# Kernel optimization log

Hardware: AMD Instinct MI355X
Metric: run time of the kernel (lower is better)

## Reference

```python
import jax, jax.numpy as jnp
import numpy as np

H = 128  # hidden size
I = 4    # input size
B = 256  # batch
T = 512  # seq len


def setup_inputs() -> dict:
    key = jax.random.key(0)
    ks = jax.random.split(key, 9)
    k = 1.0 / np.sqrt(H)  # PyTorch LSTM init: U(-1/sqrt(H), 1/sqrt(H))
    u = lambda kk, shape: jax.random.uniform(kk, shape, jnp.float32, -k, k)
    return {
        "x": jax.random.normal(ks[0], (B, T, I), jnp.float32),
        "Wih_f": u(ks[1], (4 * H, I)),
        "Whh_f": u(ks[2], (4 * H, H)),
        "bih_f": u(ks[3], (4 * H,)),
        "bhh_f": u(ks[4], (4 * H,)),
        "Wih_b": u(ks[5], (4 * H, I)),
        "Whh_b": u(ks[6], (4 * H, H)),
        "bih_b": u(ks[7], (4 * H,)),
        "bhh_b": u(ks[8], (4 * H,)),
    }


def _lstm_final_h(xt, Wih, Whh, bih, bhh):
    # xt: [T, B, I]. Returns final hidden state h_T: [B, H].
    # Precompute input projection for all timesteps (batched GEMM).
    xw = jnp.einsum("tbi,gi->tbg", xt, Wih) + (bih + bhh)  # [T, B, 4H]
    h0 = jnp.zeros((xt.shape[1], H), xt.dtype)
    c0 = jnp.zeros((xt.shape[1], H), xt.dtype)

    def step(carry, xw_t):
        h, c = carry
        gates = xw_t + h @ Whh.T  # [B, 4H]
        i, f, g, o = jnp.split(gates, 4, axis=-1)  # PyTorch gate order i,f,g,o
        i = jax.nn.sigmoid(i)
        f = jax.nn.sigmoid(f)
        g = jnp.tanh(g)
        o = jax.nn.sigmoid(o)
        c = f * c + i * g
        h = o * jnp.tanh(c)
        return (h, c), None

    (h_T, _), _ = jax.lax.scan(step, (h0, c0), xw)
    return h_T


def reference(x, Wih_f, Whh_f, bih_f, bhh_f, Wih_b, Whh_b, bih_b, bhh_b):
    xt = jnp.swapaxes(x, 0, 1)  # [T, B, I]
    h_fwd = _lstm_final_h(xt, Wih_f, Whh_f, bih_f, bhh_f)          # forward direction
    h_bwd = _lstm_final_h(xt[::-1], Wih_b, Whh_b, bih_b, bhh_b)    # backward direction
    # h_n: [2, B, H] -> transpose(0,1) -> [B, 2, H] -> reshape [B, 2H]
    return jnp.concatenate([h_fwd, h_bwd], axis=-1)
```

## Files before the change

### kernel.cpp

```cpp
#include <hip/hip_runtime.h>
#include <hip/hip_bf16.h>

typedef _Float16 f16;
typedef _Float16 f16x8 __attribute__((ext_vector_type(8)));
typedef _Float16 f16x4 __attribute__((ext_vector_type(4)));
typedef float    f32x4 __attribute__((ext_vector_type(4)));

#define HDIM 128
#define IDIM 4
#define TLEN 512

__device__ __forceinline__ float sigm(float x){
  return 1.0f / (1.0f + __expf(-x));
}
__device__ __forceinline__ float tanh_fast(float x){
  return 1.0f - 2.0f / (1.0f + __expf(2.0f*x));
}

__global__ __launch_bounds__(512, 2) void bilstm_mfma3(
    const float* __restrict__ x,
    const float* __restrict__ Wih_f, const float* __restrict__ Whh_f,
    const float* __restrict__ bih_f, const float* __restrict__ bhh_f,
    const float* __restrict__ Wih_b, const float* __restrict__ Whh_b,
    const float* __restrict__ bih_b, const float* __restrict__ bhh_b,
    float* __restrict__ out)
{
  __shared__ __align__(16) f16 xs16[2][TLEN][IDIM];
  __shared__ __align__(16) f16 ha[2][4][64][8];

  const int tid = threadIdx.x;
  const int w   = tid >> 6;
  const int l   = tid & 63;
  const int c16 = l & 15;
  const int dir = blockIdx.x >> 7;
  const int b0  = (blockIdx.x & 127) * 2;

  const float* Wih = dir ? Wih_b : Wih_f;
  const float* Whh = dir ? Whh_b : Whh_f;
  const float* bih = dir ? bih_b : bih_f;
  const float* bhh = dir ? bhh_b : bhh_f;

  f16x8 bfrag[4][5];
  #pragma unroll
  for (int t = 0; t < 4; ++t){
    const int gn = t*128 + w*16 + c16;
    #pragma unroll
    for (int ks = 0; ks < 4; ++ks){
      const float* p = Whh + gn*HDIM + ks*32 + (l>>4)*8;
      float4 qa = ((const float4*)p)[0];
      float4 qb = ((const float4*)p)[1];
      f16x8 v = { (f16)qa.x,(f16)qa.y,(f16)qa.z,(f16)qa.w,
                  (f16)qb.x,(f16)qb.y,(f16)qb.z,(f16)qb.w };
      bfrag[t][ks] = v;
    }
    f16x8 v4 = (f16x8)(f16)0.0f;
    if (l < 16){
      const float4 wq = *(const float4*)(Wih + gn*IDIM);
      const float bb = bih[gn] + bhh[gn];
      v4[0] = (f16)wq.x; v4[1] = (f16)wq.y;
      v4[2] = (f16)wq.z; v4[3] = (f16)wq.w;
      v4[4] = (f16)bb;
    }
    bfrag[t][4] = v4;
  }
  #pragma unroll
  for (int t = 0; t < 4; ++t)
    #pragma unroll
    for (int ks = 0; ks < 5; ++ks)
      asm("" : "+v"(bfrag[t][ks]));

  {
    const float4* src0 = (const float4*)(x + (size_t)(b0+0)*TLEN*IDIM);
    const float4* src1 = (const float4*)(x + (size_t)(b0+1)*TLEN*IDIM);
    float4 v0 = src0[tid], v1 = src1[tid];
    f16x4 h0 = { (f16)v0.x, (f16)v0.y, (f16)v0.z, (f16)v0.w };
    f16x4 h1 = { (f16)v1.x, (f16)v1.y, (f16)v1.z, (f16)v1.w };
    *(f16x4*)&xs16[0][tid][0] = h0;
    *(f16x4*)&xs16[1][tid][0] = h1;
  }
  {
    int* hz = (int*)ha;
    hz[tid] = 0; hz[tid+512] = 0; hz[tid+1024] = 0; hz[tid+1536] = 0;
  }
  __syncthreads();

  float c = 0.0f, hout = 0.0f;
  const int chainbit = (l >> 4) & 1;
  int tt = dir ? (TLEN-1) : 0;
  const int dt = dir ? -1 : 1;

  const int Gw  = (l >> 4) + ((2*w + (c16 >> 3)) & 3) * 16;
  const int kse = w >> 1;
  const int ew  = c16 & 7;

#define STEP(RB, WB)                                                          \
  {                                                                           \
    f16x8 a0 = *(const f16x8*)&ha[RB][0][l][0];                               \
    f16x8 a1 = *(const f16x8*)&ha[RB][1][l][0];                               \
    f16x8 a2 = *(const f16x8*)&ha[RB][2][l][0];                               \
    f16x8 a3 = *(const f16x8*)&ha[RB][3][l][0];                               \
    f16x4 xq0 = *(const f16x4*)&xs16[0][tt][0];                               \
    f16x4 xq1 = *(const f16x4*)&xs16[1][tt][0];                               \
    f16x4 zq  = (f16x4)(f16)0.0f;                                             \
    f16x4 sel = (l == 0) ? xq0 : ((l == 1) ? xq1 : zq);                       \
    f16x8 a4  = (f16x8)(f16)0.0f;                                             \
    a4[0] = sel[0]; a4[1] = sel[1]; a4[2] = sel[2]; a4[3] = sel[3];           \
    a4[4] = (l < 2) ? (f16)1.0f : (f16)0.0f;                                  \
    f32x4 zero4 = { 0.f, 0.f, 0.f, 0.f };                                     \
    f32x4 acc[4];                                                             \
    _Pragma("unroll")                                                         \
    for (int t = 0; t < 4; ++t){                                              \
      acc[t] = __builtin_amdgcn_mfma_f32_16x16x32_f16(a0, bfrag[t][0], zero4, 0,0,0); \
      acc[t] = __builtin_amdgcn_mfma_f32_16x16x32_f16(a1, bfrag[t][1], acc[t], 0,0,0); \
      acc[t] = __builtin_amdgcn_mfma_f32_16x16x32_f16(a2, bfrag[t][2], acc[t], 0,0,0); \
      acc[t] = __builtin_amdgcn_mfma_f32_16x16x32_f16(a3, bfrag[t][3], acc[t], 0,0,0); \
      acc[t] = __builtin_amdgcn_mfma_f32_16x16x32_f16(a4, bfrag[t][4], acc[t], 0,0,0); \
    }                                                                         \
    float val[4];                                                             \
    _Pragma("unroll")                                                         \
    for (int t = 0; t < 4; ++t){                                              \
      int pv = __builtin_amdgcn_ds_bpermute(c16 << 2, __float_as_int(acc[t].y)); \
      val[t] = chainbit ? __int_as_float(pv) : acc[t].x;                      \
    }                                                                         \
    float iv = sigm(val[0]);                                                  \
    float fv = sigm(val[1]);                                                  \
    float gv = tanh_fast(val[2]);                                             \
    float ov = sigm(val[3]);                                                  \
    c    = fv*c + iv*gv;                                                      \
    hout = ov * tanh_fast(c);                                                 \
    if (l < 32) ha[WB][kse][Gw][ew] = (f16)hout;                              \
    tt += dt;                                                                 \
    __syncthreads();                                                          \
  }

  for (int s = 0; s < TLEN; s += 2){
    STEP(0, 1)
    STEP(1, 0)
  }
#undef STEP

  if (l < 32){
    out[(size_t)(b0 + (l>>4))*(2*HDIM) + dir*HDIM + w*16 + c16] = hout;
  }
}

extern "C" void kernel_launch(void* const* d_in, const int* in_sizes, int n_in,
                              void* d_out, int out_size, void* d_ws, size_t ws_size,
                              hipStream_t stream)
{
  const float* x     = (const float*)d_in[0];
  const float* Wih_f = (const float*)d_in[1];
  const float* Whh_f = (const float*)d_in[2];
  const float* bih_f = (const float*)d_in[3];
  const float* bhh_f = (const float*)d_in[4];
  const float* Wih_b = (const float*)d_in[5];
  const float* Whh_b = (const float*)d_in[6];
  const float* bih_b = (const float*)d_in[7];
  const float* bhh_b = (const float*)d_in[8];

  bilstm_mfma3<<<dim3(256), dim3(512), 0, stream>>>(
      x, Wih_f, Whh_f, bih_f, bhh_f, Wih_b, Whh_b, bih_b, bhh_b,
      (float*)d_out);
}
```

Measured before the change: 437.1 us.

## Split gate tiles across 16 waves with shared-memory gate exchange

Doubles the block to 1024 threads so each wave computes two 16-column gate tiles instead of four. This halves the serial MFMA chain per step. Gate pre-activations now go through a new shared buffer and an extra barrier, so each step has two syncthreads, and the double-buffered hidden state is replaced by a single buffer. MFMA issue is raised in priority with setprio. The aim is lower per-step latency in the recurrence, paid for with an extra block-wide barrier and LDS traffic on every step.

```diff
diff --git a/kernel.cpp b/kernel.cpp
--- a/kernel.cpp
+++ b/kernel.cpp
@@ -17,7 +17,7 @@
   return 1.0f - 2.0f / (1.0f + __expf(2.0f*x));
 }
 
-__global__ __launch_bounds__(512, 2) void bilstm_mfma3(
+__global__ __launch_bounds__(1024, 4) void bilstm_v4(
     const float* __restrict__ x,
     const float* __restrict__ Wih_f, const float* __restrict__ Whh_f,
     const float* __restrict__ bih_f, const float* __restrict__ bhh_f,
@@ -26,12 +26,15 @@
     float* __restrict__ out)
 {
   __shared__ __align__(16) f16 xs16[2][TLEN][IDIM];
-  __shared__ __align__(16) f16 ha[2][4][64][8];
+  __shared__ __align__(16) f16 ha[4][64][8];
+  __shared__ __align__(16) float graw[2][8][16][4];
 
   const int tid = threadIdx.x;
-  const int w   = tid >> 6;
+  const int wid = tid >> 6;
   const int l   = tid & 63;
   const int c16 = l & 15;
+  const int p   = wid & 7;
+  const int r   = wid >> 3;
   const int dir = blockIdx.x >> 7;
   const int b0  = (blockIdx.x & 127) * 2;
 
@@ -40,18 +43,21 @@
   const float* bih = dir ? bih_b : bih_f;
   const float* bhh = dir ? bhh_b : bhh_f;
 
-  f16x8 bfrag[4][5];
+  const int t0 = p + r*16;
+  const int t1 = t0 + 8;
+
+  f16x8 bfrag[2][5];
   #pragma unroll
-  for (int t = 0; t < 4; ++t){
-    const int gn = t*128 + w*16 + c16;
+  for (int q = 0; q < 2; ++q){
+    const int gn = (q ? t1 : t0)*16 + c16;
     #pragma unroll
     for (int ks = 0; ks < 4; ++ks){
-      const float* p = Whh + gn*HDIM + ks*32 + (l>>4)*8;
-      float4 qa = ((const float4*)p)[0];
-      float4 qb = ((const float4*)p)[1];
+      const float* pp = Whh + gn*HDIM + ks*32 + (l>>4)*8;
+      float4 qa = ((const float4*)pp)[0];
+      float4 qb = ((const float4*)pp)[1];
       f16x8 v = { (f16)qa.x,(f16)qa.y,(f16)qa.z,(f16)qa.w,
                   (f16)qb.x,(f16)qb.y,(f16)qb.z,(f16)qb.w };
-      bfrag[t][ks] = v;
+      bfrag[q][ks] = v;
     }
     f16x8 v4 = (f16x8)(f16)0.0f;
     if (l < 16){
@@ -61,86 +67,83 @@
       v4[2] = (f16)wq.z; v4[3] = (f16)wq.w;
       v4[4] = (f16)bb;
     }
-    bfrag[t][4] = v4;
+    bfrag[q][4] = v4;
   }
   #pragma unroll
-  for (int t = 0; t < 4; ++t)
+  for (int q = 0; q < 2; ++q)
     #pragma unroll
     for (int ks = 0; ks < 5; ++ks)
-      asm("" : "+v"(bfrag[t][ks]));
+      asm("" : "+v"(bfrag[q][ks]));
 
   {
-    const float4* src0 = (const float4*)(x + (size_t)(b0+0)*TLEN*IDIM);
-    const float4* src1 = (const float4*)(x + (size_t)(b0+1)*TLEN*IDIM);
-    float4 v0 = src0[tid], v1 = src1[tid];
-    f16x4 h0 = { (f16)v0.x, (f16)v0.y, (f16)v0.z, (f16)v0.w };
-    f16x4 h1 = { (f16)v1.x, (f16)v1.y, (f16)v1.z, (f16)v1.w };
-    *(f16x4*)&xs16[0][tid][0] = h0;
-    *(f16x4*)&xs16[1][tid][0] = h1;
+    const int ch = tid >> 9, i = tid & 511;
+    const float4 v = ((const float4*)(x + (size_t)(b0+ch)*TLEN*IDIM))[i];
+    f16x4 hv = { (f16)v.x, (f16)v.y, (f16)v.z, (f16)v.w };
+    *(f16x4*)&xs16[ch][i][0] = hv;
   }
-  {
-    int* hz = (int*)ha;
-    hz[tid] = 0; hz[tid+512] = 0; hz[tid+1024] = 0; hz[tid+1536] = 0;
-  }
+  ((int*)ha)[tid] = 0;
   __syncthreads();
 
-  float c = 0.0f, hout = 0.0f;
-  const int chainbit = (l >> 4) & 1;
+  float cst = 0.0f, hout = 0.0f;
+
   int tt = dir ? (TLEN-1) : 0;
   const int dt = dir ? -1 : 1;
-
-  const int Gw  = (l >> 4) + ((2*w + (c16 >> 3)) & 3) * 16;
-  const int kse = w >> 1;
+  const int g0 = 2*r, g1 = 2*r + 1;
+  const int kse = p >> 1;
+  const int Gw  = r + ((2*(p&1) + (c16>>3)) & 3) * 16;
   const int ew  = c16 & 7;
 
-#define STEP(RB, WB)                                                          \
-  {                                                                           \
-    f16x8 a0 = *(const f16x8*)&ha[RB][0][l][0];                               \
-    f16x8 a1 = *(const f16x8*)&ha[RB][1][l][0];                               \
-    f16x8 a2 = *(const f16x8*)&ha[RB][2][l][0];                               \
-    f16x8 a3 = *(const f16x8*)&ha[RB][3][l][0];                               \
-    f16x4 xq0 = *(const f16x4*)&xs16[0][tt][0];                               \
-    f16x4 xq1 = *(const f16x4*)&xs16[1][tt][0];                               \
-    f16x4 zq  = (f16x4)(f16)0.0f;                                             \
-    f16x4 sel = (l == 0) ? xq0 : ((l == 1) ? xq1 : zq);                       \
-    f16x8 a4  = (f16x8)(f16)0.0f;                                             \
-    a4[0] = sel[0]; a4[1] = sel[1]; a4[2] = sel[2]; a4[3] = sel[3];           \
-    a4[4] = (l < 2) ? (f16)1.0f : (f16)0.0f;                                  \
-    f32x4 zero4 = { 0.f, 0.f, 0.f, 0.f };                                     \
-    f32x4 acc[4];                                                             \
-    _Pragma("unroll")                                                         \
-    for (int t = 0; t < 4; ++t){                                              \
-      acc[t] = __builtin_amdgcn_mfma_f32_16x16x32_f16(a0, bfrag[t][0], zero4, 0,0,0); \
-      acc[t] = __builtin_amdgcn_mfma_f32_16x16x32_f16(a1, bfrag[t][1], acc[t], 0,0,0); \
-      acc[t] = __builtin_amdgcn_mfma_f32_16x16x32_f16(a2, bfrag[t][2], acc[t], 0,0,0); \
-      acc[t] = __builtin_amdgcn_mfma_f32_16x16x32_f16(a3, bfrag[t][3], acc[t], 0,0,0); \
-      acc[t] = __builtin_amdgcn_mfma_f32_16x16x32_f16(a4, bfrag[t][4], acc[t], 0,0,0); \
-    }                                                                         \
-    float val[4];                                                             \
-    _Pragma("unroll")                                                         \
-    for (int t = 0; t < 4; ++t){                                              \
-      int pv = __builtin_amdgcn_ds_bpermute(c16 << 2, __float_as_int(acc[t].y)); \
-      val[t] = chainbit ? __int_as_float(pv) : acc[t].x;                      \
-    }                                                                         \
-    float iv = sigm(val[0]);                                                  \
-    float fv = sigm(val[1]);                                                  \
-    float gv = tanh_fast(val[2]);                                             \
-    float ov = sigm(val[3]);                                                  \
-    c    = fv*c + iv*gv;                                                      \
-    hout = ov * tanh_fast(c);                                                 \
-    if (l < 32) ha[WB][kse][Gw][ew] = (f16)hout;                              \
-    tt += dt;                                                                 \
-    __syncthreads();                                                          \
+  for (int s = 0; s < TLEN; ++s){
+    f16x8 a0 = *(const f16x8*)&ha[0][l][0];
+    f16x8 a1 = *(const f16x8*)&ha[1][l][0];
+    f16x8 a2 = *(const f16x8*)&ha[2][l][0];
+    f16x8 a3 = *(const f16x8*)&ha[3][l][0];
+    f16x4 xq0 = *(const f16x4*)&xs16[0][tt][0];
+    f16x4 xq1 = *(const f16x4*)&xs16[1][tt][0];
+    f16x4 zq  = (f16x4)(f16)0.0f;
+    f16x4 sel = (l == 0) ? xq0 : ((l == 1) ? xq1 : zq);
+    f16x8 a4  = (f16x8)(f16)0.0f;
+    a4[0] = sel[0]; a4[1] = sel[1]; a4[2] = sel[2]; a4[3] = sel[3];
+    a4[4] = (l < 2) ? (f16)1.0f : (f16)0.0f;
+
+    const f32x4 zero4 = { 0.f, 0.f, 0.f, 0.f };
+    __builtin_amdgcn_s_setprio(1);
+    f32x4 acc0 = __builtin_amdgcn_mfma_f32_16x16x32_f16(a0, bfrag[0][0], zero4, 0,0,0);
+    f32x4 acc1 = __builtin_amdgcn_mfma_f32_16x16x32_f16(a0, bfrag[1][0], zero4, 0,0,0);
+    acc0 = __builtin_amdgcn_mfma_f32_16x16x32_f16(a1, bfrag[0][1], acc0, 0,0,0);
+    acc1 = __builtin_amdgcn_mfma_f32_16x16x32_f16(a1, bfrag[1][1], acc1, 0,0,0);
+    acc0 = __builtin_amdgcn_mfma_f32_16x16x32_f16(a2, bfrag[0][2], acc0, 0,0,0);
+    acc1 = __builtin_amdgcn_mfma_f32_16x16x32_f16(a2, bfrag[1][2], acc1, 0,0,0);
+    acc0 = __builtin_amdgcn_mfma_f32_16x16x32_f16(a3, bfrag[0][3], acc0, 0,0,0);
+    acc1 = __builtin_amdgcn_mfma_f32_16x16x32_f16(a3, bfrag[1][3], acc1, 0,0,0);
+    acc0 = __builtin_amdgcn_mfma_f32_16x16x32_f16(a4, bfrag[0][4], acc0, 0,0,0);
+    acc1 = __builtin_amdgcn_mfma_f32_16x16x32_f16(a4, bfrag[1][4], acc1, 0,0,0);
+    __builtin_amdgcn_s_setprio(0);
+
+    if (l < 16){
+      graw[0][p][c16][g0] = acc0.x;
+      graw[1][p][c16][g0] = acc0.y;
+      graw[0][p][c16][g1] = acc1.x;
+      graw[1][p][c16][g1] = acc1.y;
+    }
+    __syncthreads();
+
+    if (l < 16){
+      const float4 gv = *(const float4*)&graw[r][p][c16][0];
+      float iv = sigm(gv.x);
+      float fv = sigm(gv.y);
+      float gg = tanh_fast(gv.z);
+      float ov = sigm(gv.w);
+      cst  = fv*cst + iv*gg;
+      hout = ov * tanh_fast(cst);
+      ha[kse][Gw][ew] = (f16)hout;
+    }
+    tt += dt;
+    __syncthreads();
   }
 
-  for (int s = 0; s < TLEN; s += 2){
-    STEP(0, 1)
-    STEP(1, 0)
-  }
-#undef STEP
-
-  if (l < 32){
-    out[(size_t)(b0 + (l>>4))*(2*HDIM) + dir*HDIM + w*16 + c16] = hout;
+  if (l < 16){
+    out[(size_t)(b0+r)*(2*HDIM) + dir*HDIM + p*16 + c16] = hout;
   }
 }
 
@@ -158,7 +161,7 @@
   const float* bih_b = (const float*)d_in[7];
   const float* bhh_b = (const float*)d_in[8];
 
-  bilstm_mfma3<<<dim3(256), dim3(512), 0, stream>>>(
+  bilstm_v4<<<dim3(256), dim3(1024), 0, stream>>>(
       x, Wih_f, Whh_f, bih_f, bhh_f, Wih_b, Whh_b, bih_b, bhh_b,
       (float*)d_out);
 }
```

Result: slower. 659.3 us (+50.8%).

## Drop bpermute, compute both batch rows per lane, prefetch input fragment

Applied to the files above, without the earlier changes.

Removes the per-step ds_bpermute shuffle by having lanes 0-15 compute the gate nonlinearities for both batch rows directly from acc.x and acc.y. The input/bias A fragment is built for the next step after the current step's compute, so its LDS reads come off the critical path; the bias MFMA moves first in the chain. Sigmoid and tanh now use exp2 with a hardware reciprocal, and s_setprio is raised around the MFMA block. The trade-off is that half the lanes sit idle during activations, which doubles the serial transcendental work per active lane.

```diff
diff --git a/kernel.cpp b/kernel.cpp
--- a/kernel.cpp
+++ b/kernel.cpp
@@ -10,14 +10,20 @@
 #define IDIM 4
 #define TLEN 512
 
+#if __has_builtin(__builtin_amdgcn_rcpf)
+__device__ __forceinline__ float frcp(float x){ return __builtin_amdgcn_rcpf(x); }
+#else
+__device__ __forceinline__ float frcp(float x){ return 1.0f / x; }
+#endif
+
 __device__ __forceinline__ float sigm(float x){
-  return 1.0f / (1.0f + __expf(-x));
+  return frcp(1.0f + __builtin_exp2f(x * -1.442695041f));
 }
 __device__ __forceinline__ float tanh_fast(float x){
-  return 1.0f - 2.0f / (1.0f + __expf(2.0f*x));
+  return 1.0f - 2.0f * frcp(1.0f + __builtin_exp2f(x * 2.885390082f));
 }
 
-__global__ __launch_bounds__(512, 2) void bilstm_mfma3(
+__global__ __launch_bounds__(512, 2) void bilstm_v5(
     const float* __restrict__ x,
     const float* __restrict__ Wih_f, const float* __restrict__ Whh_f,
     const float* __restrict__ bih_f, const float* __restrict__ bhh_f,
@@ -84,14 +90,29 @@
   }
   __syncthreads();
 
-  float c = 0.0f, hout = 0.0f;
-  const int chainbit = (l >> 4) & 1;
+  float c0 = 0.f, c1 = 0.f, h0o = 0.f, h1o = 0.f;
   int tt = dir ? (TLEN-1) : 0;
   const int dt = dir ? -1 : 1;
 
-  const int Gw  = (l >> 4) + ((2*w + (c16 >> 3)) & 3) * 16;
   const int kse = w >> 1;
+  const int Gw0 = ((2*w + (c16 >> 3)) & 3) * 16;
   const int ew  = c16 & 7;
+
+  const f16x4 zq = (f16x4)(f16)0.0f;
+
+#define BUILD_A4(A4, T)                                                       \
+  {                                                                           \
+    f16x4 xq0 = *(const f16x4*)&xs16[0][(T)][0];                              \
+    f16x4 xq1 = *(const f16x4*)&xs16[1][(T)][0];                              \
+    f16x4 sel = (l == 0) ? xq0 : ((l == 1) ? xq1 : zq);                       \
+    A4 = (f16x8)(f16)0.0f;                                                    \
+    A4[0] = sel[0]; A4[1] = sel[1]; A4[2] = sel[2]; A4[3] = sel[3];           \
+    A4[4] = (l < 2) ? (f16)1.0f : (f16)0.0f;                                  \
+  }
+
+  f16x8 a4;
+  BUILD_A4(a4, tt)
+  tt += dt;
 
 #define STEP(RB, WB)                                                          \
   {                                                                           \
@@ -99,36 +120,31 @@
     f16x8 a1 = *(const f16x8*)&ha[RB][1][l][0];                               \
     f16x8 a2 = *(const f16x8*)&ha[RB][2][l][0];                               \
     f16x8 a3 = *(const f16x8*)&ha[RB][3][l][0];                               \
-    f16x4 xq0 = *(const f16x4*)&xs16[0][tt][0];                               \
-    f16x4 xq1 = *(const f16x4*)&xs16[1][tt][0];                               \
-    f16x4 zq  = (f16x4)(f16)0.0f;                                             \
-    f16x4 sel = (l == 0) ? xq0 : ((l == 1) ? xq1 : zq);                       \
-    f16x8 a4  = (f16x8)(f16)0.0f;                                             \
-    a4[0] = sel[0]; a4[1] = sel[1]; a4[2] = sel[2]; a4[3] = sel[3];           \
-    a4[4] = (l < 2) ? (f16)1.0f : (f16)0.0f;                                  \
-    f32x4 zero4 = { 0.f, 0.f, 0.f, 0.f };                                     \
+    const f32x4 zero4 = { 0.f, 0.f, 0.f, 0.f };                               \
     f32x4 acc[4];                                                             \
+    __builtin_amdgcn_s_setprio(1);                                            \
     _Pragma("unroll")                                                         \
     for (int t = 0; t < 4; ++t){                                              \
-      acc[t] = __builtin_amdgcn_mfma_f32_16x16x32_f16(a0, bfrag[t][0], zero4, 0,0,0); \
+      acc[t] = __builtin_amdgcn_mfma_f32_16x16x32_f16(a4, bfrag[t][4], zero4, 0,0,0); \
+      acc[t] = __builtin_amdgcn_mfma_f32_16x16x32_f16(a0, bfrag[t][0], acc[t], 0,0,0); \
       acc[t] = __builtin_amdgcn_mfma_f32_16x16x32_f16(a1, bfrag[t][1], acc[t], 0,0,0); \
       acc[t] = __builtin_amdgcn_mfma_f32_16x16x32_f16(a2, bfrag[t][2], acc[t], 0,0,0); \
       acc[t] = __builtin_amdgcn_mfma_f32_16x16x32_f16(a3, bfrag[t][3], acc[t], 0,0,0); \
-      acc[t] = __builtin_amdgcn_mfma_f32_16x16x32_f16(a4, bfrag[t][4], acc[t], 0,0,0); \
     }                                                                         \
-    float val[4];                                                             \
-    _Pragma("unroll")                                                         \
-    for (int t = 0; t < 4; ++t){                                              \
-      int pv = __builtin_amdgcn_ds_bpermute(c16 << 2, __float_as_int(acc[t].y)); \
-      val[t] = chainbit ? __int_as_float(pv) : acc[t].x;                      \
+    __builtin_amdgcn_s_setprio(0);                                            \
+    if (l < 16){                                                              \
+      float i0 = sigm(acc[0].x), i1 = sigm(acc[0].y);                         \
+      float f0 = sigm(acc[1].x), f1 = sigm(acc[1].y);                         \
+      float g0 = tanh_fast(acc[2].x), g1 = tanh_fast(acc[2].y);               \
+      float o0 = sigm(acc[3].x), o1 = sigm(acc[3].y);                         \
+      c0 = f0*c0 + i0*g0;                                                     \
+      c1 = f1*c1 + i1*g1;                                                     \
+      h0o = o0 * tanh_fast(c0);                                               \
+      h1o = o1 * tanh_fast(c1);                                               \
+      ha[WB][kse][Gw0][ew]   = (f16)h0o;                                      \
+      ha[WB][kse][Gw0+1][ew] = (f16)h1o;                                      \
     }                                                                         \
-    float iv = sigm(val[0]);                                                  \
-    float fv = sigm(val[1]);                                                  \
-    float gv = tanh_fast(val[2]);                                             \
-    float ov = sigm(val[3]);                                                  \
-    c    = fv*c + iv*gv;                                                      \
-    hout = ov * tanh_fast(c);                                                 \
-    if (l < 32) ha[WB][kse][Gw][ew] = (f16)hout;                              \
+    BUILD_A4(a4, tt & (TLEN-1))                                               \
     tt += dt;                                                                 \
     __syncthreads();                                                          \
   }
@@ -138,9 +154,12 @@
     STEP(1, 0)
   }
 #undef STEP
+#undef BUILD_A4
 
-  if (l < 32){
-    out[(size_t)(b0 + (l>>4))*(2*HDIM) + dir*HDIM + w*16 + c16] = hout;
+  if (l < 16){
+    const int j = w*16 + c16;
+    out[(size_t)(b0+0)*(2*HDIM) + dir*HDIM + j] = h0o;
+    out[(size_t)(b0+1)*(2*HDIM) + dir*HDIM + j] = h1o;
   }
 }
 
@@ -158,7 +177,7 @@
   const float* bih_b = (const float*)d_in[7];
   const float* bhh_b = (const float*)d_in[8];
 
-  bilstm_mfma3<<<dim3(256), dim3(512), 0, stream>>>(
+  bilstm_v5<<<dim3(256), dim3(512), 0, stream>>>(
       x, Wih_f, Whh_f, bih_f, bhh_f, Wih_b, Whh_b, bih_b, bhh_b,
       (float*)d_out);
 }
```

Result: slower. 454.3 us (+3.9%).
